# Kernel optimization log

Hardware: AMD Instinct MI355X
Metric: run time of the kernel (lower is better)

The kernel has to match this reference:

```python
import jax, jax.numpy as jnp
import numpy as np

BRANCH = 16    # tree branching factor
HEIGHT = 4     # tree height (levels below virtual root 0)
D_MODEL = 1024 # feature dim of Xi / model output
IN_DIM = 1024  # raw input dim
BATCH = 4096


def _build_tree(b, h):
    # Balanced b-ary tree. Node ids are 1-based in BFS order; id 0 is the
    # virtual root (df.parent == 0 selects level-1 nodes in the original).
    level_sizes = [b ** l for l in range(1, h + 1)]
    starts = np.cumsum([1] + level_sizes)[:-1]  # first id of each level
    n_nodes = int(sum(level_sizes))
    children = np.zeros((n_nodes + 1, b), dtype=np.int32)  # 0 == no child
    children[0] = np.arange(1, b + 1)  # root's children (parent == 0)
    for l in range(1, h):
        ids = np.arange(starts[l - 1], starts[l - 1] + level_sizes[l - 1])
        pos = np.arange(level_sizes[l - 1])
        children[ids] = starts[l] + pos[:, None] * b + np.arange(b)[None, :]
    return n_nodes, children


def setup_inputs() -> dict:
    key = jax.random.key(0)
    k1, k2, k3 = jax.random.split(key, 3)
    n_nodes, children = _build_tree(BRANCH, HEIGHT)
    X = jax.random.normal(k1, (BATCH, IN_DIM), dtype=jnp.float32)
    W = jax.random.normal(k2, (IN_DIM, D_MODEL), dtype=jnp.float32) / np.sqrt(IN_DIM)
    # Xi: [d_model, n_nodes] class-embedding matrix (angle-based -> unit columns)
    Xi = jax.random.normal(k3, (D_MODEL, n_nodes), dtype=jnp.float32)
    Xi = Xi / jnp.linalg.norm(Xi, axis=0, keepdims=True)
    return {"X": X, "W": W, "Xi": Xi, "children": jnp.asarray(children)}


def reference(X, W, Xi, children):
    # f = model(X); here the stand-in model is a linear layer.
    f = X @ W                      # [B, d]
    XiT = Xi.T                     # [n_nodes, d]
    B = X.shape[0]
    neg_inf = jnp.finfo(f.dtype).min

    cur = jnp.zeros((B,), dtype=jnp.int32)          # start at virtual root 0
    cols = [jnp.zeros((B,), dtype=jnp.int32)]       # y_pred[:, 0] == 0
    for _ in range(HEIGHT):
        cand = children[cur]                         # [B, K] 1-based ids, 0 = pad
        emb = XiT[cand - 1]                          # [B, K, d] (pad rows masked below)
        g = jnp.einsum('bkd,bd->bk', emb, f)         # scores vs candidate children
        valid = cand > 0
        g = jnp.where(valid, g, neg_inf)
        idx = jnp.argmax(g, axis=-1)
        nxt = jnp.take_along_axis(cand, idx[:, None], axis=1)[:, 0]
        any_valid = jnp.any(valid, axis=-1)          # False once a leaf is reached
        nxt = jnp.where(any_valid, nxt, 0)           # original leaves y_pred at 0
        cols.append(nxt)
        cur = jnp.where(any_valid, nxt, cur)         # stop descending at leaves
    return jnp.stack(cols, axis=1)                   # [B, HEIGHT+1] int32
```

## Files before the change

### kernel.cpp

```cpp
#include <hip/hip_runtime.h>
#include <hip/hip_bf16.h>
#include <cstdint>
#include <cfloat>

#define BATCH   4096
#define IN_DIM  1024
#define D_MODEL 1024
#define BRANCH  16
#define HEIGHT  4
#define N_NODES 69904

#define BM 128
#define BN 128
#define BK 16

__global__ __launch_bounds__(256) void gemm_f32(const float* __restrict__ A,
                                                const float* __restrict__ B,
                                                float* __restrict__ C) {
    __shared__ float As[BK][BM + 4];
    __shared__ float Bs[BK][BN + 4];

    const int t  = threadIdx.x;
    const int tx = t & 15;
    const int ty = t >> 4;
    const int bm = blockIdx.x;
    const int bn = blockIdx.y;

    const int arow = t >> 2;
    const int ac4  = (t & 3) * 4;
    const int brow = t >> 5;
    const int bc4  = (t & 31) * 4;

    const float* Ab = A + (size_t)bm * BM * IN_DIM;
    const float* Bb = B + (size_t)bn * BN;

    float4 ar[2], br[2];

#define LOAD_TILE(k0)                                                          \
    {                                                                          \
        _Pragma("unroll")                                                      \
        for (int i = 0; i < 2; ++i)                                            \
            ar[i] = *(const float4*)(Ab + (size_t)(arow + 64 * i) * IN_DIM +   \
                                     (k0) + ac4);                              \
        _Pragma("unroll")                                                      \
        for (int i = 0; i < 2; ++i)                                            \
            br[i] = *(const float4*)(Bb + (size_t)((k0) + brow + 8 * i) *      \
                                     D_MODEL + bc4);                           \
    }

#define STORE_TILE()                                                           \
    {                                                                          \
        _Pragma("unroll")                                                      \
        for (int i = 0; i < 2; ++i) {                                          \
            As[ac4 + 0][arow + 64 * i] = ar[i].x;                              \
            As[ac4 + 1][arow + 64 * i] = ar[i].y;                              \
            As[ac4 + 2][arow + 64 * i] = ar[i].z;                              \
            As[ac4 + 3][arow + 64 * i] = ar[i].w;                              \
        }                                                                      \
        _Pragma("unroll")                                                      \
        for (int i = 0; i < 2; ++i)                                            \
            *(float4*)&Bs[brow + 8 * i][bc4] = br[i];                          \
    }

    float acc[8][8] = {};

#define COMPUTE_TILE()                                                         \
    {                                                                          \
        _Pragma("unroll")                                                      \
        for (int k = 0; k < BK; ++k) {                                         \
            float4 a0 = *(const float4*)&As[k][ty * 8];                        \
            float4 a1 = *(const float4*)&As[k][ty * 8 + 4];                    \
            float4 b0 = *(const float4*)&Bs[k][tx * 4];                        \
            float4 b1 = *(const float4*)&Bs[k][tx * 4 + 64];                   \
            const float aa[8] = {a0.x, a0.y, a0.z, a0.w, a1.x, a1.y, a1.z, a1.w};\
            const float bb[8] = {b0.x, b0.y, b0.z, b0.w, b1.x, b1.y, b1.z, b1.w};\
            _Pragma("unroll")                                                  \
            for (int i = 0; i < 8; ++i)                                        \
                _Pragma("unroll")                                              \
                for (int j = 0; j < 8; ++j)                                    \
                    acc[i][j] = fmaf(aa[i], bb[j], acc[i][j]);                 \
        }                                                                      \
    }

    LOAD_TILE(0);
    STORE_TILE();
    __syncthreads();

    for (int k0 = BK; k0 < IN_DIM; k0 += BK) {
        LOAD_TILE(k0);
        COMPUTE_TILE();
        __syncthreads();
        STORE_TILE();
        __syncthreads();
    }
    COMPUTE_TILE();

    float* Cb = C + (size_t)(bm * BM + ty * 8) * D_MODEL + bn * BN;
#pragma unroll
    for (int i = 0; i < 8; ++i) {
        float4 v0 = {acc[i][0], acc[i][1], acc[i][2], acc[i][3]};
        float4 v1 = {acc[i][4], acc[i][5], acc[i][6], acc[i][7]};
        *(float4*)(Cb + (size_t)i * D_MODEL + tx * 4)      = v0;
        *(float4*)(Cb + (size_t)i * D_MODEL + tx * 4 + 64) = v1;
    }
#undef LOAD_TILE
#undef STORE_TILE
#undef COMPUTE_TILE
}

__global__ __launch_bounds__(256, 6) void descend(const float* __restrict__ f,
                                                  const float* __restrict__ Xi,
                                                  const int* __restrict__ children,
                                                  int* __restrict__ out) {
    __shared__ float  fs[2][1024];
    __shared__ float4 part[2][2][4];

    const int t    = threadIdx.x;
    const int lane = t & 63;
    const int w    = t >> 6;
    const int r    = w >> 1;
    const int h    = w & 1;
    const int b    = blockIdx.x * 2 + r;

    {
        const float4* src = (const float4*)(f + (size_t)blockIdx.x * 2 * D_MODEL);
        float4* dst = (float4*)fs;
        dst[t]       = src[t];
        dst[t + 256] = src[t + 256];
    }

    const int q  = lane & 3;
    const int dg = lane >> 2;
    const float*  frd   = fs[r] + h * 512 + dg;
    const size_t  dbase = (size_t)(h * 512 + dg) * N_NODES;

    if (w == 0 && lane == 0) out[(size_t)b * (HEIGHT + 1)] = 0;
    if (w == 2 && lane == 0) out[(size_t)(b) * (HEIGHT + 1)] = 0;

    __syncthreads();

    int cur = 0;
    for (int lev = 0; lev < HEIGHT; ++lev) {
        const int child0 = __builtin_amdgcn_readfirstlane(
            children[(size_t)cur * BRANCH]);
        const float* xp = Xi + dbase + (size_t)(child0 - 1) + q * 4;

        float4 acc = {0.f, 0.f, 0.f, 0.f};
#pragma unroll 8
        for (int i = 0; i < 32; ++i) {
            float4 x  = *(const float4*)xp;
            float  fv = frd[16 * i];
            acc.x = fmaf(fv, x.x, acc.x);
            acc.y = fmaf(fv, x.y, acc.y);
            acc.z = fmaf(fv, x.z, acc.z);
            acc.w = fmaf(fv, x.w, acc.w);
            xp += (size_t)16 * N_NODES;
        }

#pragma unroll
        for (int m = 4; m <= 32; m <<= 1) {
            acc.x += __shfl_xor(acc.x, m);
            acc.y += __shfl_xor(acc.y, m);
            acc.z += __shfl_xor(acc.z, m);
            acc.w += __shfl_xor(acc.w, m);
        }
        if (lane < 4) part[r][h][lane] = acc;
        __syncthreads();

        const float4 s0 = part[r][0][q];
        const float4 s1 = part[r][1][q];
        const float sv[4] = {s0.x + s1.x, s0.y + s1.y, s0.z + s1.z, s0.w + s1.w};
        float bv = sv[0];
        int   bc = q * 4;
#pragma unroll
        for (int j = 1; j < 4; ++j)
            if (sv[j] > bv) { bv = sv[j]; bc = q * 4 + j; }
#pragma unroll
        for (int m = 1; m <= 2; m <<= 1) {
            float ov = __shfl_xor(bv, m);
            int   oc = __shfl_xor(bc, m);
            if (ov > bv || (ov == bv && oc < bc)) { bv = ov; bc = oc; }
        }

        cur = child0 + bc;
        if (h == 0 && lane == 0)
            out[(size_t)b * (HEIGHT + 1) + lev + 1] = cur;
        __syncthreads();
    }
}

extern "C" void kernel_launch(void* const* d_in, const int* in_sizes, int n_in,
                              void* d_out, int out_size, void* d_ws, size_t ws_size,
                              hipStream_t stream) {
    const float* X        = (const float*)d_in[0];
    const float* W        = (const float*)d_in[1];
    const float* Xi       = (const float*)d_in[2];
    const int*   children = (const int*)d_in[3];
    int* out = (int*)d_out;

    float* f = (float*)d_ws;

    dim3 ggrid(BATCH / BM, D_MODEL / BN);
    gemm_f32<<<ggrid, 256, 0, stream>>>(X, W, f);

    descend<<<BATCH / 2, 256, 0, stream>>>(f, Xi, children, out);
}
```

Before: 613.7 us.

## Split GEMM along K and fold partial sums into descend load

Splits the fp32 GEMM reduction dimension in two, doubling the grid so more CUs are busy, and enlarges BK to 32. The two partial outputs are summed when descend loads f into shared memory. The children table lookup is replaced by closed-form 16*cur+1 indexing for the balanced tree, removing a dependent global load per level. This costs an extra partial-output buffer write and read, and the indexing assumes the fixed balanced tree layout.

```diff
diff --git a/kernel.cpp b/kernel.cpp
--- a/kernel.cpp
+++ b/kernel.cpp
@@ -1,7 +1,5 @@
 #include <hip/hip_runtime.h>
-#include <hip/hip_bf16.h>
 #include <cstdint>
-#include <cfloat>
 
 #define BATCH   4096
 #define IN_DIM  1024
@@ -12,7 +10,8 @@
 
 #define BM 128
 #define BN 128
-#define BK 16
+#define BK 32
+#define KSPLIT 2
 
 __global__ __launch_bounds__(256) void gemm_f32(const float* __restrict__ A,
                                                 const float* __restrict__ B,
@@ -25,41 +24,48 @@
     const int ty = t >> 4;
     const int bm = blockIdx.x;
     const int bn = blockIdx.y;
+    const int kz = blockIdx.z;
 
     const int arow = t >> 2;
     const int ac4  = (t & 3) * 4;
     const int brow = t >> 5;
     const int bc4  = (t & 31) * 4;
 
-    const float* Ab = A + (size_t)bm * BM * IN_DIM;
-    const float* Bb = B + (size_t)bn * BN;
-
-    float4 ar[2], br[2];
+    const float* Ab = A + (size_t)bm * BM * IN_DIM + (size_t)kz * 512;
+    const float* Bb = B + (size_t)kz * 512 * D_MODEL + (size_t)bn * BN;
+
+    float4 ar[2][2], br[2][2];
 
 #define LOAD_TILE(k0)                                                          \
     {                                                                          \
         _Pragma("unroll")                                                      \
-        for (int i = 0; i < 2; ++i)                                            \
-            ar[i] = *(const float4*)(Ab + (size_t)(arow + 64 * i) * IN_DIM +   \
-                                     (k0) + ac4);                              \
-        _Pragma("unroll")                                                      \
-        for (int i = 0; i < 2; ++i)                                            \
-            br[i] = *(const float4*)(Bb + (size_t)((k0) + brow + 8 * i) *      \
-                                     D_MODEL + bc4);                           \
+        for (int s = 0; s < 2; ++s) {                                          \
+            _Pragma("unroll")                                                  \
+            for (int i = 0; i < 2; ++i)                                        \
+                ar[s][i] = *(const float4*)(Ab + (size_t)(arow + 64 * i) *     \
+                                            IN_DIM + (k0) + 16 * s + ac4);     \
+            _Pragma("unroll")                                                  \
+            for (int i = 0; i < 2; ++i)                                        \
+                br[s][i] = *(const float4*)(Bb + (size_t)((k0) + 16 * s +      \
+                                            brow + 8 * i) * D_MODEL + bc4);    \
+        }                                                                      \
     }
 
 #define STORE_TILE()                                                           \
     {                                                                          \
         _Pragma("unroll")                                                      \
-        for (int i = 0; i < 2; ++i) {                                          \
-            As[ac4 + 0][arow + 64 * i] = ar[i].x;                              \
-            As[ac4 + 1][arow + 64 * i] = ar[i].y;                              \
-            As[ac4 + 2][arow + 64 * i] = ar[i].z;                              \
-            As[ac4 + 3][arow + 64 * i] = ar[i].w;                              \
+        for (int s = 0; s < 2; ++s) {                                          \
+            _Pragma("unroll")                                                  \
+            for (int i = 0; i < 2; ++i) {                                      \
+                As[16 * s + ac4 + 0][arow + 64 * i] = ar[s][i].x;              \
+                As[16 * s + ac4 + 1][arow + 64 * i] = ar[s][i].y;              \
+                As[16 * s + ac4 + 2][arow + 64 * i] = ar[s][i].z;              \
+                As[16 * s + ac4 + 3][arow + 64 * i] = ar[s][i].w;              \
+            }                                                                  \
+            _Pragma("unroll")                                                  \
+            for (int i = 0; i < 2; ++i)                                        \
+                *(float4*)&Bs[16 * s + brow + 8 * i][bc4] = br[s][i];          \
         }                                                                      \
-        _Pragma("unroll")                                                      \
-        for (int i = 0; i < 2; ++i)                                            \
-            *(float4*)&Bs[brow + 8 * i][bc4] = br[i];                          \
     }
 
     float acc[8][8] = {};
@@ -86,7 +92,7 @@
     STORE_TILE();
     __syncthreads();
 
-    for (int k0 = BK; k0 < IN_DIM; k0 += BK) {
+    for (int k0 = BK; k0 < 512; k0 += BK) {
         LOAD_TILE(k0);
         COMPUTE_TILE();
         __syncthreads();
@@ -95,7 +101,8 @@
     }
     COMPUTE_TILE();
 
-    float* Cb = C + (size_t)(bm * BM + ty * 8) * D_MODEL + bn * BN;
+    float* Cb = C + (size_t)kz * BATCH * D_MODEL +
+                (size_t)(bm * BM + ty * 8) * D_MODEL + bn * BN;
 #pragma unroll
     for (int i = 0; i < 8; ++i) {
         float4 v0 = {acc[i][0], acc[i][1], acc[i][2], acc[i][3]};
@@ -110,7 +117,6 @@
 
 __global__ __launch_bounds__(256, 6) void descend(const float* __restrict__ f,
                                                   const float* __restrict__ Xi,
-                                                  const int* __restrict__ children,
                                                   int* __restrict__ out) {
     __shared__ float  fs[2][1024];
     __shared__ float4 part[2][2][4];
@@ -123,10 +129,16 @@
     const int b    = blockIdx.x * 2 + r;
 
     {
-        const float4* src = (const float4*)(f + (size_t)blockIdx.x * 2 * D_MODEL);
+        const float4* s0 = (const float4*)(f + (size_t)blockIdx.x * 2 * D_MODEL);
+        const float4* s1 = s0 + ((size_t)BATCH * D_MODEL) / 4;
         float4* dst = (float4*)fs;
-        dst[t]       = src[t];
-        dst[t + 256] = src[t + 256];
+#pragma unroll
+        for (int i = 0; i < 2; ++i) {
+            float4 a = s0[t + 256 * i];
+            float4 c = s1[t + 256 * i];
+            float4 v = {a.x + c.x, a.y + c.y, a.z + c.z, a.w + c.w};
+            dst[t + 256 * i] = v;
+        }
     }
 
     const int q  = lane & 3;
@@ -134,15 +146,13 @@
     const float*  frd   = fs[r] + h * 512 + dg;
     const size_t  dbase = (size_t)(h * 512 + dg) * N_NODES;
 
-    if (w == 0 && lane == 0) out[(size_t)b * (HEIGHT + 1)] = 0;
-    if (w == 2 && lane == 0) out[(size_t)(b) * (HEIGHT + 1)] = 0;
+    if ((w == 0 || w == 2) && lane == 0) out[(size_t)b * (HEIGHT + 1)] = 0;
 
     __syncthreads();
 
     int cur = 0;
     for (int lev = 0; lev < HEIGHT; ++lev) {
-        const int child0 = __builtin_amdgcn_readfirstlane(
-            children[(size_t)cur * BRANCH]);
+        const int child0 = 16 * cur + 1;
         const float* xp = Xi + dbase + (size_t)(child0 - 1) + q * 4;
 
         float4 acc = {0.f, 0.f, 0.f, 0.f};
@@ -192,16 +202,15 @@
 extern "C" void kernel_launch(void* const* d_in, const int* in_sizes, int n_in,
                               void* d_out, int out_size, void* d_ws, size_t ws_size,
                               hipStream_t stream) {
-    const float* X        = (const float*)d_in[0];
-    const float* W        = (const float*)d_in[1];
-    const float* Xi       = (const float*)d_in[2];
-    const int*   children = (const int*)d_in[3];
+    const float* X  = (const float*)d_in[0];
+    const float* W  = (const float*)d_in[1];
+    const float* Xi = (const float*)d_in[2];
     int* out = (int*)d_out;
 
     float* f = (float*)d_ws;
 
-    dim3 ggrid(BATCH / BM, D_MODEL / BN);
+    dim3 ggrid(BATCH / BM, D_MODEL / BN, KSPLIT);
     gemm_f32<<<ggrid, 256, 0, stream>>>(X, W, f);
 
-    descend<<<BATCH / 2, 256, 0, stream>>>(f, Xi, children, out);
+    descend<<<BATCH / 2, 256, 0, stream>>>(f, Xi, out);
 }
```

New measurement: 626.5 us. +2.1%, slower.
